# Kernel optimization log

Hardware: AMD Instinct MI355X
Metric: run time of the kernel (lower is better)

## Reference

```python
import jax, jax.numpy as jnp
from jax import lax
import numpy as np

NPOINT = 1024
RADIUS = 0.2
NSAMPLE = 32
MLP = [64, 64, 128]
EPS = 1e-5  # BatchNorm eps (torch default)


def setup_inputs() -> dict:
    key = jax.random.key(0)
    ks = jax.random.split(key, 2 + 3 * len(MLP))
    B, N = 8, 16384
    d = {
        "xyz": jax.random.uniform(ks[0], (B, N, 3), dtype=jnp.float32),
        "points": jax.random.normal(ks[1], (B, N, 3), dtype=jnp.float32),
    }
    cin = 6  # 3 (relative xyz) + 3 (point features)
    for i, cout in enumerate(MLP):
        d[f"w{i}"] = jax.random.normal(ks[2 + i], (cout, cin), dtype=jnp.float32) / np.float32(np.sqrt(cin))
        d[f"b{i}"] = jnp.zeros((cout,), jnp.float32)
        d[f"g{i}"] = jnp.ones((cout,), jnp.float32)
        d[f"be{i}"] = jnp.zeros((cout,), jnp.float32)
        cin = cout
    return d


def _fps(xyz, npoint):
    """Farthest point sampling. xyz: (B,N,3) -> idx (B,npoint) int32.
    Deterministic start at index 0 (original uses a random start)."""
    B, N, _ = xyz.shape

    def step(carry, _):
        distance, farthest = carry  # (B,N), (B,)
        centroid = jnp.take_along_axis(xyz, farthest[:, None, None], axis=1)  # (B,1,3)
        dist = jnp.sum((xyz - centroid) ** 2, axis=-1)  # (B,N)
        distance = jnp.minimum(distance, dist)
        nxt = jnp.argmax(distance, axis=-1).astype(jnp.int32)
        return (distance, nxt), farthest

    init = (jnp.full((B, N), 1e10, xyz.dtype), jnp.zeros((B,), jnp.int32))
    _, idxs = lax.scan(step, init, None, length=npoint)
    return idxs.T  # (B, npoint)


def _gather(points, idx):
    """points: (B,N,C), idx: (B,...) -> (B,...,C)."""
    return jax.vmap(lambda p, i: p[i])(points, idx)


def _ball_query(radius, nsample, xyz, new_xyz):
    B, N, _ = xyz.shape
    # (B,S,N) pairwise squared distances
    sqr = jnp.sum((new_xyz[:, :, None, :] - xyz[:, None, :, :]) ** 2, axis=-1)
    gidx = jnp.where(sqr > radius * radius, N, jnp.arange(N, dtype=jnp.int32))
    gidx = jnp.sort(gidx, axis=-1)[:, :, :nsample]  # (B,S,K)
    # replace out-of-ball (==N) with first in-ball index
    gidx = jnp.where(gidx == N, gidx[:, :, :1], gidx)
    return gidx


def reference(xyz, points, w0, b0, g0, be0, w1, b1, g1, be1, w2, b2, g2, be2):
    B, N, _ = xyz.shape
    fidx = _fps(xyz, NPOINT)                      # (B,S)
    new_xyz = _gather(xyz, fidx)                  # (B,S,3)
    gidx = _ball_query(RADIUS, NSAMPLE, xyz, new_xyz)  # (B,S,K)
    grouped_xyz = _gather(xyz, gidx) - new_xyz[:, :, None, :]  # (B,S,K,3)
    grouped_pts = _gather(points, gidx)           # (B,S,K,C)
    feat = jnp.concatenate([grouped_xyz, grouped_pts], axis=-1)  # (B,S,K,6)
    # shared MLP = 1x1 Conv2d + BatchNorm2d(train-mode stats) + ReLU
    for w, b, g, be in ((w0, b0, g0, be0), (w1, b1, g1, be1), (w2, b2, g2, be2)):
        feat = jnp.einsum('bskc,oc->bsko', feat, w) + b
        mu = feat.mean(axis=(0, 1, 2))
        var = feat.var(axis=(0, 1, 2))  # biased, as torch BN uses for normalization
        feat = jax.nn.relu(g * (feat - mu) * lax.rsqrt(var + EPS) + be)
    new_points = feat.max(axis=2)                 # max over nsample -> (B,S,C_out)
    return new_xyz, new_points
```

## Files before the change

kernel.cpp:

```cpp
#include <hip/hip_runtime.h>
#include <stdint.h>

#pragma clang fp contract(off)

#define NPT   16384
#define BB    8
#define SS    1024
#define KSAMP 32
#define PTOT  (BB*SS*KSAMP)
#define NGRP  (BB*SS)
#define R2    0.04f
#define EPSBN 1e-5f
#define INV_M 3.814697265625e-06f

#define OFF_S1 0
#define OFF_Q1 64
#define OFF_S2 128
#define OFF_Q2 192
#define OFF_S3 256
#define OFF_Q3 384
#define OFF_A1 512
#define OFF_C1 576
#define OFF_A2 640
#define OFF_C2 704
#define OFF_A3 768
#define OFF_C3 896
#define OFF_ZMAX 1024
#define OFF_FEAT (1024 + 1048576)

__device__ __forceinline__ float wave_sum(float v) {
#pragma unroll
  for (int off = 32; off; off >>= 1) v += __shfl_xor(v, off);
  return v;
}

__device__ __forceinline__ float wave_max_dpp(float x) {
  int v = __float_as_int(x), t;
  t = __builtin_amdgcn_update_dpp(0, v, 0x111, 0xf, 0xf, true);
  v = __float_as_int(fmaxf(__int_as_float(v), __int_as_float(t)));
  t = __builtin_amdgcn_update_dpp(0, v, 0x112, 0xf, 0xf, true);
  v = __float_as_int(fmaxf(__int_as_float(v), __int_as_float(t)));
  t = __builtin_amdgcn_update_dpp(0, v, 0x114, 0xf, 0xf, true);
  v = __float_as_int(fmaxf(__int_as_float(v), __int_as_float(t)));
  t = __builtin_amdgcn_update_dpp(0, v, 0x118, 0xf, 0xf, true);
  v = __float_as_int(fmaxf(__int_as_float(v), __int_as_float(t)));
  t = __builtin_amdgcn_update_dpp(0, v, 0x142, 0xf, 0xf, true);
  v = __float_as_int(fmaxf(__int_as_float(v), __int_as_float(t)));
  t = __builtin_amdgcn_update_dpp(0, v, 0x143, 0xf, 0xf, true);
  v = __float_as_int(fmaxf(__int_as_float(v), __int_as_float(t)));
  return __int_as_float(__builtin_amdgcn_readlane(v, 63));
}

__device__ __forceinline__ unsigned wave_min_u32_dpp(unsigned x) {
  unsigned v = x, t;
  t = (unsigned)__builtin_amdgcn_update_dpp(-1, (int)v, 0x111, 0xf, 0xf, false);
  v = v < t ? v : t;
  t = (unsigned)__builtin_amdgcn_update_dpp(-1, (int)v, 0x112, 0xf, 0xf, false);
  v = v < t ? v : t;
  t = (unsigned)__builtin_amdgcn_update_dpp(-1, (int)v, 0x114, 0xf, 0xf, false);
  v = v < t ? v : t;
  t = (unsigned)__builtin_amdgcn_update_dpp(-1, (int)v, 0x118, 0xf, 0xf, false);
  v = v < t ? v : t;
  t = (unsigned)__builtin_amdgcn_update_dpp(-1, (int)v, 0x142, 0xf, 0xf, false);
  v = v < t ? v : t;
  t = (unsigned)__builtin_amdgcn_update_dpp(-1, (int)v, 0x143, 0xf, 0xf, false);
  v = v < t ? v : t;
  return (unsigned)__builtin_amdgcn_readlane((int)v, 63);
}

__device__ __forceinline__ float wave_sum_dpp(float x) {
  float v = x;
  int t;
  t = __builtin_amdgcn_update_dpp(0, __float_as_int(v), 0x111, 0xf, 0xf, true);
  v += __int_as_float(t);
  t = __builtin_amdgcn_update_dpp(0, __float_as_int(v), 0x112, 0xf, 0xf, true);
  v += __int_as_float(t);
  t = __builtin_amdgcn_update_dpp(0, __float_as_int(v), 0x114, 0xf, 0xf, true);
  v += __int_as_float(t);
  t = __builtin_amdgcn_update_dpp(0, __float_as_int(v), 0x118, 0xf, 0xf, true);
  v += __int_as_float(t);
  t = __builtin_amdgcn_update_dpp(0, __float_as_int(v), 0x142, 0xf, 0xf, true);
  v += __int_as_float(t);
  t = __builtin_amdgcn_update_dpp(0, __float_as_int(v), 0x143, 0xf, 0xf, true);
  v += __int_as_float(t);
  return __int_as_float(__builtin_amdgcn_readlane(__float_as_int(v), 63));
}

__device__ __forceinline__ void half_max_dpp(float x, float& lo, float& hi) {
  int v = __float_as_int(x), t;
  t = __builtin_amdgcn_update_dpp(v, v, 0x111, 0xf, 0xf, false);
  v = __float_as_int(fmaxf(__int_as_float(v), __int_as_float(t)));
  t = __builtin_amdgcn_update_dpp(v, v, 0x112, 0xf, 0xf, false);
  v = __float_as_int(fmaxf(__int_as_float(v), __int_as_float(t)));
  t = __builtin_amdgcn_update_dpp(v, v, 0x114, 0xf, 0xf, false);
  v = __float_as_int(fmaxf(__int_as_float(v), __int_as_float(t)));
  t = __builtin_amdgcn_update_dpp(v, v, 0x118, 0xf, 0xf, false);
  v = __float_as_int(fmaxf(__int_as_float(v), __int_as_float(t)));
  t = __builtin_amdgcn_update_dpp(v, v, 0x142, 0xf, 0xf, false);
  v = __float_as_int(fmaxf(__int_as_float(v), __int_as_float(t)));
  lo = __int_as_float(__builtin_amdgcn_readlane(v, 31));
  hi = __int_as_float(__builtin_amdgcn_readlane(v, 63));
}

__global__ __launch_bounds__(1024)
void fps_kernel(const float* __restrict__ xyz, float* __restrict__ newxyz) {
  extern __shared__ float smem[];
  float2* sxy = (float2*)smem;
  __shared__ unsigned long long wkey[2];
  __shared__ float cpub[2];
  const int b = blockIdx.x;
  const int t = threadIdx.x;
  const int lane = t & 63;
  const float* xb = xyz + (size_t)b * NPT * 3;

  float z[16], d[16];
#pragma unroll
  for (int j = 0; j < 16; ++j) {
    int p = j * 1024 + t;
    float xx = xb[3 * p];
    float yy = xb[3 * p + 1];
    float zz = xb[3 * p + 2];
    sxy[p] = make_float2(xx, yy);
    z[j] = zz;
    d[j] = 1e10f;
    asm volatile("" : "+v"(z[j]));
  }

  float cx = xb[0], cy = xb[1], cz = xb[2];
  if (t == 0) {
    wkey[0] = 0ull; wkey[1] = 0ull;
    float* o = newxyz + (size_t)b * SS * 3;
    o[0] = cx; o[1] = cy; o[2] = cz;
  }
  __syncthreads();

  const float2* pA = sxy + t;
  const float2* pB = sxy + t + 8192;

  for (int it = 1; it < SS; ++it) {
    const int buf = it & 1;
    float bv = 0.0f;
#pragma unroll
    for (int j = 0; j < 16; ++j) {
      float2 xy = (j < 8) ? pA[j * 1024] : pB[(j - 8) * 1024];
      float dx = xy.x - cx, dy = xy.y - cy, dz = z[j] - cz;
      float d2 = (dx * dx + dy * dy) + dz * dz;
      float dm = fminf(d[j], d2);
      d[j] = dm;
      bv = fmaxf(bv, dm);
    }
    const float wm = wave_max_dpp(bv);

    unsigned cand = 0xffffffffu;
    float zc = 0.0f;
    if (bv == wm) {
      int bj = 0;
#pragma unroll
      for (int j = 15; j >= 0; --j) {
        if (d[j] == wm) { bj = j; zc = z[j]; }
      }
      cand = (unsigned)(bj * 1024 + t);
    }
    const unsigned wmin = wave_min_u32_dpp(cand);
    if (lane == 0)
      atomicMax(&wkey[buf],
                ((unsigned long long)__float_as_uint(wm) << 32) |
                (unsigned long long)(unsigned)~wmin);
    __syncthreads();
    const unsigned long long k = wkey[buf];
    int fi = (int)~(unsigned)k;
    fi = __builtin_amdgcn_readfirstlane(fi);
    if (t == 0) wkey[buf ^ 1] = 0ull;
    if (cand == (unsigned)fi) cpub[buf] = zc;
    float2 cxy = sxy[fi];
    cx = cxy.x; cy = cxy.y;
    __syncthreads();
    cz = cpub[buf];
    if (t == 0) {
      float* o = newxyz + ((size_t)b * SS + it) * 3;
      o[0] = cx; o[1] = cy; o[2] = cz;
    }
  }
}

__global__ __launch_bounds__(256, 2)
void ballq_kernel(const float* __restrict__ xyz, const float* __restrict__ pts,
                  const float* __restrict__ newxyz, float* __restrict__ feat) {
  const int lane = threadIdx.x & 63;
  const int c = blockIdx.x * 4 + (threadIdx.x >> 6);
  const int b = c >> 10;
  const float* xb = xyz + (size_t)b * NPT * 3;
  const float* pb = pts + (size_t)b * NPT * 3;
  const float cx = newxyz[3 * c], cy = newxyz[3 * c + 1], cz = newxyz[3 * c + 2];
  const int base = c * KSAMP;
  const uint64_t ltm = (1ull << lane) - 1ull;

  int cnt = 0, firstp = 0;
  bool haveFirst = false;
  for (int p0 = 0; p0 < NPT && cnt < KSAMP; p0 += 64) {
    int p = p0 + lane;
    float px = xb[3 * p], py = xb[3 * p + 1], pz = xb[3 * p + 2];
    float dx = cx - px, dy = cy - py, dz = cz - pz;
    float sqr = (dx * dx + dy * dy) + dz * dz;
    bool in = (sqr <= R2);
    uint64_t m = __ballot(in);
    if (!haveFirst && m) { firstp = p0 + (__ffsll((unsigned long long)m) - 1); haveFirst = true; }
    int rank = (int)__popcll(m & ltm);
    int slot = cnt + rank;
    if (in && slot < KSAMP) {
      int idx = base + slot;
      feat[0 * PTOT + idx] = px - cx;
      feat[1 * PTOT + idx] = py - cy;
      feat[2 * PTOT + idx] = pz - cz;
      feat[3 * PTOT + idx] = pb[3 * p];
      feat[4 * PTOT + idx] = pb[3 * p + 1];
      feat[5 * PTOT + idx] = pb[3 * p + 2];
    }
    cnt += (int)__popcll(m);
  }
  if (cnt < KSAMP) {
    int slot = cnt + lane;
    if (slot < KSAMP) {
      int idx = base + slot;
      float px = xb[3 * firstp], py = xb[3 * firstp + 1], pz = xb[3 * firstp + 2];
      feat[0 * PTOT + idx] = px - cx;
      feat[1 * PTOT + idx] = py - cy;
      feat[2 * PTOT + idx] = pz - cz;
      feat[3 * PTOT + idx] = pb[3 * firstp];
      feat[4 * PTOT + idx] = pb[3 * firstp + 1];
      feat[5 * PTOT + idx] = pb[3 * firstp + 2];
    }
  }
}

__global__ __launch_bounds__(256, 2)
void mlp1s_kernel(const float* __restrict__ feat, const float* __restrict__ w0,
                  const float* __restrict__ b0, float* __restrict__ stats) {
  float s[64], q[64];
#pragma unroll
  for (int o = 0; o < 64; ++o) { s[o] = 0.0f; q[o] = 0.0f; }
  int gid = blockIdx.x * 256 + threadIdx.x;
  for (int p = gid; p < PTOT; p += 256 * 256) {
    float f[6];
#pragma unroll
    for (int ch = 0; ch < 6; ++ch) f[ch] = feat[ch * PTOT + p];
#pragma unroll
    for (int o = 0; o < 64; ++o) {
      float z = b0[o];
#pragma unroll
      for (int i = 0; i < 6; ++i) z = fmaf(w0[o * 6 + i], f[i], z);
      s[o] += z; q[o] = fmaf(z, z, q[o]);
    }
  }
  const int lane = threadIdx.x & 63;
#pragma unroll
  for (int o = 0; o < 64; ++o) { s[o] = wave_sum(s[o]); q[o] = wave_sum(q[o]); }
  __shared__ float ls[128];
  if (threadIdx.x < 128) ls[threadIdx.x] = 0.0f;
  __syncthreads();
  if (lane == 0) {
#pragma unroll
    for (int o = 0; o < 64; ++o) { atomicAdd(&ls[o], s[o]); atomicAdd(&ls[64 + o], q[o]); }
  }
  __syncthreads();
  if (threadIdx.x < 64) atomicAdd(&stats[OFF_S1 + threadIdx.x], ls[threadIdx.x]);
  else if (threadIdx.x < 128) atomicAdd(&stats[OFF_Q1 + threadIdx.x - 64], ls[threadIdx.x]);
}

__global__ void fin_kernel(const float* __restrict__ g, const float* __restrict__ be,
                           const float* __restrict__ s, const float* __restrict__ q,
                           float* __restrict__ A, float* __restrict__ C, int Cn) {
  int o = blockIdx.x * blockDim.x + threadIdx.x;
  if (o >= Cn) return;
  float mu = s[o] * INV_M;
  float var = q[o] * INV_M - mu * mu;
  float a = g[o] / sqrtf(var + EPSBN);
  A[o] = a;
  C[o] = be[o] - a * mu;
}

__global__ __launch_bounds__(256, 2)
void mlp2s_kernel(const float* __restrict__ feat,
                  const float* __restrict__ w0, const float* __restrict__ b0,
                  const float* __restrict__ w1, const float* __restrict__ b1,
                  const float* __restrict__ par, float* __restrict__ stats) {
  const float* a1 = par + OFF_A1;
  const float* c1 = par + OFF_C1;
  const int lane = threadIdx.x & 63;
  float sp = 0.0f, qp = 0.0f;
  int gid = blockIdx.x * 256 + threadIdx.x;
  for (int p = gid; p < PTOT; p += 512 * 256) {
    float f[6];
#pragma unroll
    for (int ch = 0; ch < 6; ++ch) f[ch] = feat[ch * PTOT + p];
    float h1[64];
#pragma unroll
    for (int o = 0; o < 64; ++o) {
      float z = b0[o];
#pragma unroll
      for (int i = 0; i < 6; ++i) z = fmaf(w0[o * 6 + i], f[i], z);
      h1[o] = fmaxf(fmaf(a1[o], z, c1[o]), 0.0f);
    }
    for (int o = 0; o < 64; o += 2) {
      float z0 = b1[o], z1 = b1[o + 1];
#pragma unroll
      for (int i = 0; i < 64; ++i) {
        z0 = fmaf(w1[o * 64 + i], h1[i], z0);
        z1 = fmaf(w1[(o + 1) * 64 + i], h1[i], z1);
      }
      float s0 = wave_sum_dpp(z0), q0 = wave_sum_dpp(z0 * z0);
      float s1 = wave_sum_dpp(z1), q1 = wave_sum_dpp(z1 * z1);
      if (lane == o)     { sp += s0; qp += q0; }
      if (lane == o + 1) { sp += s1; qp += q1; }
    }
  }
  atomicAdd(&stats[OFF_S2 + lane], sp);
  atomicAdd(&stats[OFF_Q2 + lane], qp);
}

__global__ __launch_bounds__(256, 2)
void mlp3f_kernel(const float* __restrict__ feat,
                  const float* __restrict__ w0, const float* __restrict__ b0,
                  const float* __restrict__ w1, const float* __restrict__ b1,
                  const float* __restrict__ w2, const float* __restrict__ b2,
                  const float* __restrict__ par, float* __restrict__ stats,
                  float* __restrict__ zmax) {
  const float* a1 = par + OFF_A1;
  const float* c1 = par + OFF_C1;
  const float* a2 = par + OFF_A2;
  const float* c2 = par + OFF_C2;
  const int lane = threadIdx.x & 63;
  float sp0 = 0.0f, qp0 = 0.0f;
  float sp1 = 0.0f, qp1 = 0.0f;
  int gid = blockIdx.x * 256 + threadIdx.x;
  for (int p = gid; p < PTOT; p += 512 * 256) {
    float f[6];
#pragma unroll
    for (int ch = 0; ch < 6; ++ch) f[ch] = feat[ch * PTOT + p];
    float h2[64];
#pragma unroll
    for (int o = 0; o < 64; ++o) h2[o] = b1[o];
    for (int i = 0; i < 64; ++i) {
      float z = b0[i];
#pragma unroll
      for (int ch = 0; ch < 6; ++ch) z = fmaf(w0[i * 6 + ch], f[ch], z);
      float h1i = fmaxf(fmaf(a1[i], z, c1[i]), 0.0f);
#pragma unroll
      for (int o = 0; o < 64; ++o) h2[o] = fmaf(w1[o * 64 + i], h1i, h2[o]);
    }
#pragma unroll
    for (int o = 0; o < 64; ++o) h2[o] = fmaxf(fmaf(a2[o], h2[o], c2[o]), 0.0f);

    const int g = p >> 5;
    for (int o = 0; o < 128; o += 2) {
      float z0 = b2[o], z1 = b2[o + 1];
#pragma unroll
      for (int i = 0; i < 64; ++i) {
        z0 = fmaf(w2[o * 64 + i], h2[i], z0);
        z1 = fmaf(w2[(o + 1) * 64 + i], h2[i], z1);
      }
      float s0 = wave_sum_dpp(z0), q0 = wave_sum_dpp(z0 * z0);
      float s1 = wave_sum_dpp(z1), q1 = wave_sum_dpp(z1 * z1);
      if (lane == (o & 63))       { if (o < 64) { sp0 += s0; qp0 += q0; } else { sp1 += s0; qp1 += q0; } }
      if (lane == ((o + 1) & 63)) { if (o < 64) { sp0 += s1; qp0 += q1; } else { sp1 += s1; qp1 += q1; } }
      float m0lo, m0hi, m1lo, m1hi;
      half_max_dpp(z0, m0lo, m0hi);
      half_max_dpp(z1, m1lo, m1hi);
      if ((lane & 31) == (o & 31))
        zmax[g * 128 + o]     = (lane < 32) ? m0lo : m0hi;
      if ((lane & 31) == ((o + 1) & 31))
        zmax[g * 128 + o + 1] = (lane < 32) ? m1lo : m1hi;
    }
  }
  atomicAdd(&stats[OFF_S3 + lane], sp0);
  atomicAdd(&stats[OFF_Q3 + lane], qp0);
  atomicAdd(&stats[OFF_S3 + 64 + lane], sp1);
  atomicAdd(&stats[OFF_Q3 + 64 + lane], qp1);
}

__global__ __launch_bounds__(256, 4)
void final_out_kernel(const float* __restrict__ zmax, const float* __restrict__ par,
                      float* __restrict__ out2) {
  const float* a3 = par + OFF_A3;
  const float* c3 = par + OFF_C3;
  int idx = blockIdx.x * 256 + threadIdx.x;
  int c = idx & 127;
  out2[idx] = fmaxf(fmaf(a3[c], zmax[idx], c3[c]), 0.0f);
}

extern "C" void kernel_launch(void* const* d_in, const int* in_sizes, int n_in,
                              void* d_out, int out_size, void* d_ws, size_t ws_size,
                              hipStream_t stream) {
  const float* xyz = (const float*)d_in[0];
  const float* pts = (const float*)d_in[1];
  const float* w0  = (const float*)d_in[2];
  const float* b0  = (const float*)d_in[3];
  const float* g0  = (const float*)d_in[4];
  const float* be0 = (const float*)d_in[5];
  const float* w1  = (const float*)d_in[6];
  const float* b1  = (const float*)d_in[7];
  const float* g1  = (const float*)d_in[8];
  const float* be1 = (const float*)d_in[9];
  const float* w2  = (const float*)d_in[10];
  const float* b2  = (const float*)d_in[11];
  const float* g2  = (const float*)d_in[12];
  const float* be2 = (const float*)d_in[13];

  float* out  = (float*)d_out;
  float* nxz  = out;
  float* out2 = out + BB * SS * 3;

  float* ws    = (float*)d_ws;
  float* stats = ws;
  float* par   = ws;
  float* zmax  = ws + OFF_ZMAX;
  float* feat  = ws + OFF_FEAT;

  hipMemsetAsync(stats, 0, 512 * sizeof(float), stream);

  fps_kernel<<<BB, 1024, NPT * sizeof(float2), stream>>>(xyz, nxz);
  ballq_kernel<<<2048, 256, 0, stream>>>(xyz, pts, nxz, feat);

  mlp1s_kernel<<<256, 256, 0, stream>>>(feat, w0, b0, stats);
  fin_kernel<<<1, 64, 0, stream>>>(g0, be0, stats + OFF_S1, stats + OFF_Q1,
                                   par + OFF_A1, par + OFF_C1, 64);
  mlp2s_kernel<<<512, 256, 0, stream>>>(feat, w0, b0, w1, b1, par, stats);
  fin_kernel<<<1, 64, 0, stream>>>(g1, be1, stats + OFF_S2, stats + OFF_Q2,
                                   par + OFF_A2, par + OFF_C2, 64);
  mlp3f_kernel<<<512, 256, 0, stream>>>(feat, w0, b0, w1, b1, w2, b2, par, stats, zmax);
  fin_kernel<<<1, 128, 0, stream>>>(g2, be2, stats + OFF_S3, stats + OFF_Q3,
                                    par + OFF_A3, par + OFF_C3, 128);
  final_out_kernel<<<4096, 256, 0, stream>>>(zmax, par, out2);
}
```

Baseline: 2.616 ms.

## Batch FPS LDS loads before compute and revert MLP reductions to shuffles

In the farthest-point-sampling loop, all 16 shared-memory xy loads are now issued up front and fenced with a scheduling barrier, and the kernel is pinned to four waves per EU. The intent is to hide LDS latency in the serial 1023-iteration loop. The MLP stat kernels also swap the DPP-based wave sum and half-max reductions back to __shfl_xor loops, which are simpler but likely cost more instructions per reduction.

```diff
diff --git a/kernel.cpp b/kernel.cpp
--- a/kernel.cpp
+++ b/kernel.cpp
@@ -33,6 +33,11 @@
   for (int off = 32; off; off >>= 1) v += __shfl_xor(v, off);
   return v;
 }
+__device__ __forceinline__ float half_max(float v) {
+#pragma unroll
+  for (int off = 16; off; off >>= 1) v = fmaxf(v, __shfl_xor(v, off));
+  return v;
+}
 
 __device__ __forceinline__ float wave_max_dpp(float x) {
   int v = __float_as_int(x), t;
@@ -68,41 +73,8 @@
   return (unsigned)__builtin_amdgcn_readlane((int)v, 63);
 }
 
-__device__ __forceinline__ float wave_sum_dpp(float x) {
-  float v = x;
-  int t;
-  t = __builtin_amdgcn_update_dpp(0, __float_as_int(v), 0x111, 0xf, 0xf, true);
-  v += __int_as_float(t);
-  t = __builtin_amdgcn_update_dpp(0, __float_as_int(v), 0x112, 0xf, 0xf, true);
-  v += __int_as_float(t);
-  t = __builtin_amdgcn_update_dpp(0, __float_as_int(v), 0x114, 0xf, 0xf, true);
-  v += __int_as_float(t);
-  t = __builtin_amdgcn_update_dpp(0, __float_as_int(v), 0x118, 0xf, 0xf, true);
-  v += __int_as_float(t);
-  t = __builtin_amdgcn_update_dpp(0, __float_as_int(v), 0x142, 0xf, 0xf, true);
-  v += __int_as_float(t);
-  t = __builtin_amdgcn_update_dpp(0, __float_as_int(v), 0x143, 0xf, 0xf, true);
-  v += __int_as_float(t);
-  return __int_as_float(__builtin_amdgcn_readlane(__float_as_int(v), 63));
-}
-
-__device__ __forceinline__ void half_max_dpp(float x, float& lo, float& hi) {
-  int v = __float_as_int(x), t;
-  t = __builtin_amdgcn_update_dpp(v, v, 0x111, 0xf, 0xf, false);
-  v = __float_as_int(fmaxf(__int_as_float(v), __int_as_float(t)));
-  t = __builtin_amdgcn_update_dpp(v, v, 0x112, 0xf, 0xf, false);
-  v = __float_as_int(fmaxf(__int_as_float(v), __int_as_float(t)));
-  t = __builtin_amdgcn_update_dpp(v, v, 0x114, 0xf, 0xf, false);
-  v = __float_as_int(fmaxf(__int_as_float(v), __int_as_float(t)));
-  t = __builtin_amdgcn_update_dpp(v, v, 0x118, 0xf, 0xf, false);
-  v = __float_as_int(fmaxf(__int_as_float(v), __int_as_float(t)));
-  t = __builtin_amdgcn_update_dpp(v, v, 0x142, 0xf, 0xf, false);
-  v = __float_as_int(fmaxf(__int_as_float(v), __int_as_float(t)));
-  lo = __int_as_float(__builtin_amdgcn_readlane(v, 31));
-  hi = __int_as_float(__builtin_amdgcn_readlane(v, 63));
-}
-
 __global__ __launch_bounds__(1024)
+__attribute__((amdgpu_waves_per_eu(4, 4)))
 void fps_kernel(const float* __restrict__ xyz, float* __restrict__ newxyz) {
   extern __shared__ float smem[];
   float2* sxy = (float2*)smem;
@@ -139,11 +111,18 @@
 
   for (int it = 1; it < SS; ++it) {
     const int buf = it & 1;
+
+    float2 xy[16];
+#pragma unroll
+    for (int j = 0; j < 8; ++j) xy[j] = pA[j * 1024];
+#pragma unroll
+    for (int j = 8; j < 16; ++j) xy[j] = pB[(j - 8) * 1024];
+    __builtin_amdgcn_sched_barrier(0);
+
     float bv = 0.0f;
 #pragma unroll
     for (int j = 0; j < 16; ++j) {
-      float2 xy = (j < 8) ? pA[j * 1024] : pB[(j - 8) * 1024];
-      float dx = xy.x - cx, dy = xy.y - cy, dz = z[j] - cz;
+      float dx = xy[j].x - cx, dy = xy[j].y - cy, dz = z[j] - cz;
       float d2 = (dx * dx + dy * dy) + dz * dz;
       float dm = fminf(d[j], d2);
       d[j] = dm;
@@ -308,8 +287,8 @@
         z0 = fmaf(w1[o * 64 + i], h1[i], z0);
         z1 = fmaf(w1[(o + 1) * 64 + i], h1[i], z1);
       }
-      float s0 = wave_sum_dpp(z0), q0 = wave_sum_dpp(z0 * z0);
-      float s1 = wave_sum_dpp(z1), q1 = wave_sum_dpp(z1 * z1);
+      float s0 = wave_sum(z0), q0 = wave_sum(z0 * z0);
+      float s1 = wave_sum(z1), q1 = wave_sum(z1 * z1);
       if (lane == o)     { sp += s0; qp += q0; }
       if (lane == o + 1) { sp += s1; qp += q1; }
     }
@@ -359,17 +338,13 @@
         z0 = fmaf(w2[o * 64 + i], h2[i], z0);
         z1 = fmaf(w2[(o + 1) * 64 + i], h2[i], z1);
       }
-      float s0 = wave_sum_dpp(z0), q0 = wave_sum_dpp(z0 * z0);
-      float s1 = wave_sum_dpp(z1), q1 = wave_sum_dpp(z1 * z1);
+      float s0 = wave_sum(z0), q0 = wave_sum(z0 * z0);
+      float s1 = wave_sum(z1), q1 = wave_sum(z1 * z1);
       if (lane == (o & 63))       { if (o < 64) { sp0 += s0; qp0 += q0; } else { sp1 += s0; qp1 += q0; } }
       if (lane == ((o + 1) & 63)) { if (o < 64) { sp0 += s1; qp0 += q1; } else { sp1 += s1; qp1 += q1; } }
-      float m0lo, m0hi, m1lo, m1hi;
-      half_max_dpp(z0, m0lo, m0hi);
-      half_max_dpp(z1, m1lo, m1hi);
-      if ((lane & 31) == (o & 31))
-        zmax[g * 128 + o]     = (lane < 32) ? m0lo : m0hi;
-      if ((lane & 31) == ((o + 1) & 31))
-        zmax[g * 128 + o + 1] = (lane < 32) ? m1lo : m1hi;
+      float m0 = half_max(z0), m1 = half_max(z1);
+      if ((lane & 31) == (o & 31))       zmax[g * 128 + o]     = m0;
+      if ((lane & 31) == ((o + 1) & 31)) zmax[g * 128 + o + 1] = m1;
     }
   }
   atomicAdd(&stats[OFF_S3 + lane], sp0);
```

Measured after the change: 2.610 ms. Within noise of the previous version (-0.2%).
